# Kernel tuning notes

Measured on AMD Instinct MI355X. Metric: run time of the kernel, lower is better.

Reference implementation:

```python
import jax, jax.numpy as jnp
import numpy as np

B, T, D = 32, 2048, 256   # batch, encoder time steps, input_dim
H = 256                   # output_dim (GRU hidden)
A = 128                   # attention_dim
C = 4367                  # nb_classes
STEPS = 22                # max_out_t_steps


def setup_inputs() -> dict:
    key = jax.random.key(0)
    ks = jax.random.split(key, 11)
    s = 0.05
    return {
        "x": jax.random.normal(ks[0], (B, T, D), dtype=jnp.float32),
        # additive attention params: softmax_T(tanh(x Wx + h Wh) @ v)
        "Wx": jax.random.normal(ks[1], (D, A), dtype=jnp.float32) * s,
        "Wh": jax.random.normal(ks[2], (H, A), dtype=jnp.float32) * s,
        "v": jax.random.normal(ks[3], (A,), dtype=jnp.float32) * s,
        # torch GRUCell params
        "W_ih": jax.random.normal(ks[4], (3 * H, D), dtype=jnp.float32) * s,
        "W_hh": jax.random.normal(ks[5], (3 * H, H), dtype=jnp.float32) * s,
        "b_ih": jax.random.normal(ks[6], (3 * H,), dtype=jnp.float32) * s,
        "b_hh": jax.random.normal(ks[7], (3 * H,), dtype=jnp.float32) * s,
        # classifier
        "W_cls": jax.random.normal(ks[8], (C, H), dtype=jnp.float32) * s,
        "b_cls": jax.random.normal(ks[9], (C,), dtype=jnp.float32) * s,
    }


def reference(x, Wx, Wh, v, W_ih, W_hh, b_ih, b_hh, W_cls, b_cls):
    # dropout layers are identity in eval/reference mode
    xW = jnp.einsum("btd,da->bta", x, Wx)  # hoisted: constant across steps
    h0 = jnp.zeros((x.shape[0], H), dtype=x.dtype)

    def step(h, _):
        # additive attention over time axis
        e = jnp.einsum("bta,a->bt", jnp.tanh(xW + (h @ Wh)[:, None, :]), v)
        att = jax.nn.softmax(e, axis=1)          # [B, T]
        ctx = jnp.einsum("btd,bt->bd", x, att)   # weighted sum over T
        # torch GRUCell
        gi = ctx @ W_ih.T + b_ih                  # [B, 3H]
        gh = h @ W_hh.T + b_hh                    # [B, 3H]
        i_r, i_z, i_n = jnp.split(gi, 3, axis=1)
        h_r, h_z, h_n = jnp.split(gh, 3, axis=1)
        r = jax.nn.sigmoid(i_r + h_r)
        z = jax.nn.sigmoid(i_z + h_z)
        n = jnp.tanh(i_n + r * h_n)
        h_new = (1.0 - z) * n + z * h
        logits = h_new @ W_cls.T + b_cls          # [B, C]
        return h_new, logits

    _, outs = jax.lax.scan(step, h0, None, length=STEPS)  # [STEPS, B, C]
    return jnp.transpose(outs, (1, 0, 2))                 # [B, STEPS, C]
```

## Files before the change

### kernel.cpp

```cpp
#include <hip/hip_runtime.h>

#define BB 32
#define TT 2048
#define DD 256
#define HH 256
#define AA 128
#define CC 4367
#define CLS_LD 4480
#define NSTEPS 22
#define NCHUNK 32

typedef unsigned short ushortT;
typedef unsigned int uintT;
typedef unsigned long long u64T;
using frag8 = __attribute__((ext_vector_type(8))) short;
using f32x4 = __attribute__((ext_vector_type(4))) float;

__device__ __forceinline__ float tanh_fast(float u) {
  float e = __expf(2.0f * u);
  return 1.0f - 2.0f / (e + 1.0f);
}
__device__ __forceinline__ float sigmoid_fast(float u) {
  return 1.0f / (1.0f + __expf(-u));
}
__device__ __forceinline__ ushortT f2bf(float f) {
  unsigned int u = __float_as_uint(f);
  unsigned int r = (u + 0x7FFFu + ((u >> 16) & 1u)) >> 16;
  return (ushortT)r;
}
__device__ __forceinline__ float bf2f(ushortT v) {
  return __uint_as_float(((unsigned int)v) << 16);
}

__global__ __launch_bounds__(256) void trans_kernel(
    const float* __restrict__ Wx, const float* __restrict__ W_cls,
    float* __restrict__ WclsT, ushortT* __restrict__ WxT_bf) {
  int blk = blockIdx.x;
  __shared__ float tile[32][33];
  const int li = threadIdx.x >> 5, lj = threadIdx.x & 31;
  if (blk < 1096) {
    int i0 = (blk >> 3) * 32, j0 = (blk & 7) * 32;
#pragma unroll
    for (int k = 0; k < 4; ++k) {
      int i = i0 + li + k * 8;
      if (i < CC) tile[li + k * 8][lj] = W_cls[(size_t)i * 256 + j0 + lj];
    }
    __syncthreads();
#pragma unroll
    for (int k = 0; k < 4; ++k) {
      int j = j0 + li + k * 8, i = i0 + lj;
      if (i < CC) WclsT[(size_t)j * CLS_LD + i] = tile[lj][li + k * 8];
    }
  } else {
    blk -= 1096;
    int i0 = (blk >> 2) * 32, j0 = (blk & 3) * 32;
#pragma unroll
    for (int k = 0; k < 4; ++k)
      tile[li + k * 8][lj] = Wx[(size_t)(i0 + li + k * 8) * 128 + j0 + lj];
    __syncthreads();
#pragma unroll
    for (int k = 0; k < 4; ++k) {
      int j = j0 + li + k * 8;
      WxT_bf[(size_t)j * 256 + i0 + lj] = f2bf(tile[lj][li + k * 8]);
    }
  }
}

__global__ __launch_bounds__(256) void xw_mfma(
    const float* __restrict__ x, const ushortT* __restrict__ WxT_bf,
    ushortT* __restrict__ x_bf, ushortT* __restrict__ xWT) {
  __shared__ ushortT lds[2 * 128 * 72];
#define SX(r, c) lds[(r) * 72 + (c)]
#define SW(r, c) lds[128 * 72 + (r) * 72 + (c)]
#define ST(a, m) lds[(a) * 136 + (m)]
  const int tid = threadIdx.x;
  const int lane = tid & 63, w = tid >> 6;
  const int l15 = lane & 15, quad = lane >> 4;
  const int r0 = blockIdx.x * 128;
  const int bb = blockIdx.x >> 4, t0 = (blockIdx.x & 15) * 128;
  const int row = tid >> 1, half = tid & 1;

  f32x4 acc[2][8];
#pragma unroll
  for (int mt = 0; mt < 2; ++mt)
#pragma unroll
    for (int nt = 0; nt < 8; ++nt) acc[mt][nt] = (f32x4){0.f, 0.f, 0.f, 0.f};

  for (int kk0 = 0; kk0 < 256; kk0 += 64) {
    {
      const float4* xp = (const float4*)(x + (size_t)(r0 + row) * DD + kk0 + half * 32);
      uint4 pk[4];
#pragma unroll
      for (int i = 0; i < 4; ++i) {
        float4 f0 = xp[2 * i], f1 = xp[2 * i + 1];
        pk[i].x = (uintT)f2bf(f0.x) | ((uintT)f2bf(f0.y) << 16);
        pk[i].y = (uintT)f2bf(f0.z) | ((uintT)f2bf(f0.w) << 16);
        pk[i].z = (uintT)f2bf(f1.x) | ((uintT)f2bf(f1.y) << 16);
        pk[i].w = (uintT)f2bf(f1.z) | ((uintT)f2bf(f1.w) << 16);
      }
      uint4* sxp = (uint4*)&SX(row, half * 32);
      uint4* gxp = (uint4*)(x_bf + (size_t)(r0 + row) * DD + kk0 + half * 32);
#pragma unroll
      for (int i = 0; i < 4; ++i) { sxp[i] = pk[i]; gxp[i] = pk[i]; }
    }
    {
      const uint4* wp = (const uint4*)(WxT_bf + (size_t)row * DD + kk0 + half * 32);
      uint4* swp = (uint4*)&SW(row, half * 32);
#pragma unroll
      for (int i = 0; i < 4; ++i) swp[i] = wp[i];
    }
    __syncthreads();
#pragma unroll
    for (int kk = 0; kk < 2; ++kk) {
      frag8 a0 = *(const frag8*)&SX(w * 32 + l15, kk * 32 + quad * 8);
      frag8 a1 = *(const frag8*)&SX(w * 32 + 16 + l15, kk * 32 + quad * 8);
#pragma unroll
      for (int nt = 0; nt < 8; ++nt) {
        frag8 bf = *(const frag8*)&SW(nt * 16 + l15, kk * 32 + quad * 8);
        acc[0][nt] = __builtin_amdgcn_mfma_f32_16x16x32_bf16(a0, bf, acc[0][nt], 0, 0, 0);
        acc[1][nt] = __builtin_amdgcn_mfma_f32_16x16x32_bf16(a1, bf, acc[1][nt], 0, 0, 0);
      }
    }
    __syncthreads();
  }
#pragma unroll
  for (int mt = 0; mt < 2; ++mt)
#pragma unroll
    for (int nt = 0; nt < 8; ++nt)
#pragma unroll
      for (int r = 0; r < 4; ++r) {
        int m = w * 32 + mt * 16 + quad * 4 + r;
        int a = nt * 16 + l15;
        ST(a, m) = f2bf(acc[mt][nt][r]);
      }
  __syncthreads();
  {
    const uint4* sp = (const uint4*)&ST(row, half * 64);
    uint4* gp = (uint4*)(xWT + ((size_t)bb * AA + row) * TT + t0 + half * 64);
#pragma unroll
    for (int i = 0; i < 8; ++i) gp[i] = sp[i];
  }
#undef SX
#undef SW
#undef ST
}

__global__ __launch_bounds__(256) void gates_kernel(
    const float* __restrict__ ctx_part, const float* __restrict__ den_part,
    const float* __restrict__ hall, const float* __restrict__ W_ih,
    const float* __restrict__ W_hh, const float* __restrict__ b_ih,
    const float* __restrict__ b_hh, float* __restrict__ gi_buf,
    float* __restrict__ gh_buf, int s) {
  const int slice = blockIdx.x, b = blockIdx.y, tid = threadIdx.x;
  __shared__ __align__(16) float sctx[DD];
  __shared__ float sden;
  if (tid < 32) {
    float d = den_part[b * NCHUNK + tid];
#pragma unroll
    for (int off = 16; off > 0; off >>= 1) d += __shfl_down(d, off, 32);
    if (tid == 0) sden = d;
  }
  {
    float acc = 0.f;
#pragma unroll
    for (int c = 0; c < NCHUNK; ++c)
      acc += ctx_part[((size_t)b * NCHUNK + c) * DD + tid];
    sctx[tid] = acc;
  }
  __syncthreads();
  const float invd = 1.0f / sden;
  const int kq = tid & 15, gsub = tid >> 4;
  const float4* cp = (const float4*)sctx + kq * 4;
  const float4* hrow = (s >= 2) ? (const float4*)(hall + ((size_t)(s - 2) * BB + b) * HH) + kq * 4 : nullptr;
  float4 c4[4], h4[4];
#pragma unroll
  for (int j = 0; j < 4; ++j) {
    float4 cv = cp[j];
    c4[j].x = cv.x * invd; c4[j].y = cv.y * invd; c4[j].z = cv.z * invd; c4[j].w = cv.w * invd;
    if (hrow) h4[j] = hrow[j];
    else { h4[j].x = 0.f; h4[j].y = 0.f; h4[j].z = 0.f; h4[j].w = 0.f; }
  }
#pragma unroll
  for (int it = 0; it < 3; ++it) {
    const int g = slice * 48 + it * 16 + gsub;
    const float4* wi = (const float4*)(W_ih + (size_t)g * DD) + kq * 4;
    const float4* wh = (const float4*)(W_hh + (size_t)g * HH) + kq * 4;
    float gi = 0.f, gh = 0.f;
#pragma unroll
    for (int j = 0; j < 4; ++j) {
      float4 wv = wi[j];
      gi += c4[j].x * wv.x + c4[j].y * wv.y + c4[j].z * wv.z + c4[j].w * wv.w;
      wv = wh[j];
      gh += h4[j].x * wv.x + h4[j].y * wv.y + h4[j].z * wv.z + h4[j].w * wv.w;
    }
#pragma unroll
    for (int off = 8; off > 0; off >>= 1) {
      gi += __shfl_down(gi, off, 16);
      gh += __shfl_down(gh, off, 16);
    }
    if (kq == 0) {
      gi_buf[b * 768 + g] = gi + b_ih[g];
      gh_buf[b * 768 + g] = gh + b_hh[g];
    }
  }
}

__global__ __launch_bounds__(256) void hcomb_kernel(
    const float* __restrict__ gi_buf, const float* __restrict__ gh_buf,
    const float* __restrict__ Wh, float* __restrict__ hall,
    float* __restrict__ hWh_buf, int s) {
  const int b = blockIdx.x, as = blockIdx.y, i = threadIdx.x;
  __shared__ float sh[HH];
  __shared__ float part[8][32];
  {
    float gir = gi_buf[b * 768 + i], giz = gi_buf[b * 768 + 256 + i], gin = gi_buf[b * 768 + 512 + i];
    float ghr = gh_buf[b * 768 + i], ghz = gh_buf[b * 768 + 256 + i], ghn = gh_buf[b * 768 + 512 + i];
    float hp = (s >= 2) ? hall[((size_t)(s - 2) * BB + b) * HH + i] : 0.f;
    float r = sigmoid_fast(gir + ghr);
    float z = sigmoid_fast(giz + ghz);
    float n = tanh_fast(gin + r * ghn);
    float hv = (1.f - z) * n + z * hp;
    if (as == 0) hall[((size_t)(s - 1) * BB + b) * HH + i] = hv;
    sh[i] = hv;
  }
  __syncthreads();
  {
    const int a = i & 31, kq = i >> 5;
    const int ga = as * 32 + a;
    float acc = 0.f;
#pragma unroll
    for (int k = kq * 32; k < kq * 32 + 32; ++k)
      acc = fmaf(sh[k], Wh[k * AA + ga], acc);
    part[kq][a] = acc;
  }
  __syncthreads();
  if (i < 32) {
    float sum = part[0][i] + part[1][i] + part[2][i] + part[3][i]
              + part[4][i] + part[5][i] + part[6][i] + part[7][i];
    hWh_buf[b * AA + as * 32 + i] = sum;
  }
}

__global__ __launch_bounds__(256, 4) void att_kernel(
    const ushortT* __restrict__ x_bf, const ushortT* __restrict__ xWT_bf,
    const float* __restrict__ hWh_buf, const float* __restrict__ v,
    float* __restrict__ ctx_part, float* __restrict__ den_part) {
  const int tid = threadIdx.x;
  const int b = blockIdx.x;
  const int chunk = blockIdx.y;
  const int t0 = chunk * 64;
  __shared__ float sh_hWh[AA], sh_v[AA];
  __shared__ float sh_part[8 * 64];
  __shared__ float sh_w[64];
  __shared__ __align__(16) float sh_ctx[4 * DD];
  if (tid < AA) {
    sh_hWh[tid] = hWh_buf ? hWh_buf[b * AA + tid] : 0.f;
    sh_v[tid] = v[tid];
  }
  const int j4 = tid >> 6, dq = tid & 63;
  u64T xr[16];
  {
    const u64T* xb4 = (const u64T*)x_bf;
#pragma unroll
    for (int j = 0; j < 16; ++j)
      xr[j] = __builtin_nontemporal_load(
          &xb4[(((size_t)(b * TT + t0 + j * 4 + j4)) * DD >> 2) + dq]);
  }
  __syncthreads();
  {
    const int q = tid >> 5, tp = tid & 31;
    float p0 = 0.f, p1 = 0.f;
    const ushort2* xw2 = (const ushort2*)xWT_bf;
    const size_t base = (size_t)b * (AA * TT / 2) + (t0 >> 1) + tp;
#pragma unroll
    for (int i = 0; i < 16; ++i) {
      int a = q * 16 + i;
      ushort2 u = xw2[base + (size_t)a * (TT / 2)];
      float hwa = sh_hWh[a], va = sh_v[a];
      p0 = fmaf(tanh_fast(bf2f(u.x) + hwa), va, p0);
      p1 = fmaf(tanh_fast(bf2f(u.y) + hwa), va, p1);
    }
    sh_part[q * 64 + 2 * tp] = p0;
    sh_part[q * 64 + 2 * tp + 1] = p1;
  }
  __syncthreads();
  if (tid < 64) {
    float e = 0.f;
#pragma unroll
    for (int q = 0; q < 8; ++q) e += sh_part[q * 64 + tid];
    sh_w[tid] = __expf(e);
  }
  __syncthreads();
  {
    float4 acc = {0.f, 0.f, 0.f, 0.f};
#pragma unroll
    for (int j = 0; j < 16; ++j) {
      float w = sh_w[j * 4 + j4];
      u64T u = xr[j];
      acc.x = fmaf(w, bf2f((ushortT)(u       & 0xFFFFu)), acc.x);
      acc.y = fmaf(w, bf2f((ushortT)((u >> 16) & 0xFFFFu)), acc.y);
      acc.z = fmaf(w, bf2f((ushortT)((u >> 32) & 0xFFFFu)), acc.z);
      acc.w = fmaf(w, bf2f((ushortT)((u >> 48) & 0xFFFFu)), acc.w);
    }
    ((float4*)sh_ctx)[j4 * 64 + dq] = acc;
  }
  __syncthreads();
  {
    float sum = sh_ctx[tid] + sh_ctx[DD + tid] + sh_ctx[2 * DD + tid] + sh_ctx[3 * DD + tid];
    ctx_part[((size_t)b * NCHUNK + chunk) * DD + tid] = sum;
  }
  if (tid < 64) {
    float ds = sh_w[tid];
#pragma unroll
    for (int off = 32; off > 0; off >>= 1) ds += __shfl_down(ds, off, 64);
    if (tid == 0) den_part[b * NCHUNK + chunk] = ds;
  }
}

__global__ __launch_bounds__(256) void cls_kernel(
    const float* __restrict__ hall, const float* __restrict__ WclsT,
    const float* __restrict__ b_cls, float* __restrict__ out) {
  const int tid = threadIdx.x;
  const int c0 = blockIdx.x * 128;
  const int r0 = blockIdx.y * 32;
  const int cq = tid & 31, rg = tid >> 5;
  const int c = c0 + cq * 4;
  __shared__ __align__(16) float shh[32 * HH];
  {
    const float4* hsrc = (const float4*)(hall + (size_t)r0 * HH);
    float4* hdst = (float4*)shh;
#pragma unroll
    for (int i = 0; i < 8; ++i) hdst[tid + 256 * i] = hsrc[tid + 256 * i];
  }
  __syncthreads();
  float acc[4][4];
#pragma unroll
  for (int j = 0; j < 4; ++j)
#pragma unroll
    for (int l = 0; l < 4; ++l) acc[j][l] = 0.f;
#pragma unroll 4
  for (int k = 0; k < HH; ++k) {
    float4 w4 = *(const float4*)(WclsT + (size_t)k * CLS_LD + c);
    float h0 = shh[(rg * 4 + 0) * HH + k];
    float h1 = shh[(rg * 4 + 1) * HH + k];
    float h2 = shh[(rg * 4 + 2) * HH + k];
    float h3 = shh[(rg * 4 + 3) * HH + k];
    acc[0][0] = fmaf(h0, w4.x, acc[0][0]); acc[0][1] = fmaf(h0, w4.y, acc[0][1]);
    acc[0][2] = fmaf(h0, w4.z, acc[0][2]); acc[0][3] = fmaf(h0, w4.w, acc[0][3]);
    acc[1][0] = fmaf(h1, w4.x, acc[1][0]); acc[1][1] = fmaf(h1, w4.y, acc[1][1]);
    acc[1][2] = fmaf(h1, w4.z, acc[1][2]); acc[1][3] = fmaf(h1, w4.w, acc[1][3]);
    acc[2][0] = fmaf(h2, w4.x, acc[2][0]); acc[2][1] = fmaf(h2, w4.y, acc[2][1]);
    acc[2][2] = fmaf(h2, w4.z, acc[2][2]); acc[2][3] = fmaf(h2, w4.w, acc[2][3]);
    acc[3][0] = fmaf(h3, w4.x, acc[3][0]); acc[3][1] = fmaf(h3, w4.y, acc[3][1]);
    acc[3][2] = fmaf(h3, w4.z, acc[3][2]); acc[3][3] = fmaf(h3, w4.w, acc[3][3]);
  }
#pragma unroll
  for (int j = 0; j < 4; ++j) {
    int row = r0 + rg * 4 + j;
    int bb = row & (BB - 1), st = row >> 5;
    size_t obase = ((size_t)bb * NSTEPS + st) * CC;
#pragma unroll
    for (int l = 0; l < 4; ++l) {
      int cc = c + l;
      if (cc < CC) out[obase + cc] = acc[j][l] + b_cls[cc];
    }
  }
}

extern "C" void kernel_launch(void* const* d_in, const int* in_sizes, int n_in,
                              void* d_out, int out_size, void* d_ws, size_t ws_size,
                              hipStream_t stream) {
  const float* x     = (const float*)d_in[0];
  const float* Wx    = (const float*)d_in[1];
  const float* Wh    = (const float*)d_in[2];
  const float* v     = (const float*)d_in[3];
  const float* W_ih  = (const float*)d_in[4];
  const float* W_hh  = (const float*)d_in[5];
  const float* b_ih  = (const float*)d_in[6];
  const float* b_hh  = (const float*)d_in[7];
  const float* W_cls = (const float*)d_in[8];
  const float* b_cls = (const float*)d_in[9];
  float* out = (float*)d_out;

  float* ctx_part = (float*)d_ws;
  float* den_part = ctx_part + (size_t)BB * NCHUNK * DD;
  float* hWh_buf  = den_part + BB * NCHUNK;
  float* gi_buf   = hWh_buf + BB * AA;
  float* gh_buf   = gi_buf + BB * 768;
  float* hall     = gh_buf + BB * 768;
  float* WclsT    = hall + (size_t)NSTEPS * BB * HH;
  ushortT* WxT_bf = (ushortT*)(WclsT + (size_t)256 * CLS_LD);
  ushortT* x_bf   = WxT_bf + 128 * 256;
  ushortT* xWT    = x_bf + (size_t)BB * TT * DD;

  trans_kernel<<<1096 + 32, 256, 0, stream>>>(Wx, W_cls, WclsT, WxT_bf);
  xw_mfma<<<(BB * TT) / 128, 256, 0, stream>>>(x, WxT_bf, x_bf, xWT);

  att_kernel<<<dim3(BB, NCHUNK), 256, 0, stream>>>(x_bf, xWT, nullptr, v, ctx_part, den_part);
  for (int s = 1; s < NSTEPS; ++s) {
    gates_kernel<<<dim3(16, BB), 256, 0, stream>>>(ctx_part, den_part, hall, W_ih, W_hh,
                                                   b_ih, b_hh, gi_buf, gh_buf, s);
    hcomb_kernel<<<dim3(BB, 4), 256, 0, stream>>>(gi_buf, gh_buf, Wh, hall, hWh_buf, s);
    att_kernel<<<dim3(BB, NCHUNK), 256, 0, stream>>>(x_bf, xWT, hWh_buf, v, ctx_part, den_part);
  }
  gates_kernel<<<dim3(16, BB), 256, 0, stream>>>(ctx_part, den_part, hall, W_ih, W_hh,
                                                 b_ih, b_hh, gi_buf, gh_buf, NSTEPS);
  hcomb_kernel<<<dim3(BB, 4), 256, 0, stream>>>(gi_buf, gh_buf, Wh, hall, hWh_buf, NSTEPS);
  cls_kernel<<<dim3(35, 22), 256, 0, stream>>>(hall, WclsT, b_cls, out);
}
```

Measured before the change: 690.6 us.

## Fuse GRU combine and h·Wh projection into attention kernel; shrink classifier tiles

Removes the per-step hcomb kernel launch. Each attention block now recomputes the GRU hidden-state update and the h·Wh projection redundantly per chunk, overlapping it with its x loads. Only chunk 0 writes h back to global memory. The classifier kernel processes 16 rows per block instead of 32, doubling the grid for more parallelism. In exchange, the full 256x128 Wh matvec is recomputed in all 32 chunks per batch row, which adds redundant compute and L2 traffic.

```diff
diff --git a/kernel.cpp b/kernel.cpp
--- a/kernel.cpp
+++ b/kernel.cpp
@@ -207,44 +207,24 @@
 
 __global__ __launch_bounds__(256) void hcomb_kernel(
     const float* __restrict__ gi_buf, const float* __restrict__ gh_buf,
-    const float* __restrict__ Wh, float* __restrict__ hall,
-    float* __restrict__ hWh_buf, int s) {
-  const int b = blockIdx.x, as = blockIdx.y, i = threadIdx.x;
-  __shared__ float sh[HH];
-  __shared__ float part[8][32];
-  {
-    float gir = gi_buf[b * 768 + i], giz = gi_buf[b * 768 + 256 + i], gin = gi_buf[b * 768 + 512 + i];
-    float ghr = gh_buf[b * 768 + i], ghz = gh_buf[b * 768 + 256 + i], ghn = gh_buf[b * 768 + 512 + i];
-    float hp = (s >= 2) ? hall[((size_t)(s - 2) * BB + b) * HH + i] : 0.f;
-    float r = sigmoid_fast(gir + ghr);
-    float z = sigmoid_fast(giz + ghz);
-    float n = tanh_fast(gin + r * ghn);
-    float hv = (1.f - z) * n + z * hp;
-    if (as == 0) hall[((size_t)(s - 1) * BB + b) * HH + i] = hv;
-    sh[i] = hv;
-  }
-  __syncthreads();
-  {
-    const int a = i & 31, kq = i >> 5;
-    const int ga = as * 32 + a;
-    float acc = 0.f;
-#pragma unroll
-    for (int k = kq * 32; k < kq * 32 + 32; ++k)
-      acc = fmaf(sh[k], Wh[k * AA + ga], acc);
-    part[kq][a] = acc;
-  }
-  __syncthreads();
-  if (i < 32) {
-    float sum = part[0][i] + part[1][i] + part[2][i] + part[3][i]
-              + part[4][i] + part[5][i] + part[6][i] + part[7][i];
-    hWh_buf[b * AA + as * 32 + i] = sum;
-  }
+    float* __restrict__ hall, int s) {
+  const int b = blockIdx.x, i = threadIdx.x;
+  float gir = gi_buf[b * 768 + i], giz = gi_buf[b * 768 + 256 + i], gin = gi_buf[b * 768 + 512 + i];
+  float ghr = gh_buf[b * 768 + i], ghz = gh_buf[b * 768 + 256 + i], ghn = gh_buf[b * 768 + 512 + i];
+  float hp = (s >= 2) ? hall[((size_t)(s - 2) * BB + b) * HH + i] : 0.f;
+  float r = sigmoid_fast(gir + ghr);
+  float z = sigmoid_fast(giz + ghz);
+  float n = tanh_fast(gin + r * ghn);
+  float hv = (1.f - z) * n + z * hp;
+  hall[((size_t)(s - 1) * BB + b) * HH + i] = hv;
 }
 
 __global__ __launch_bounds__(256, 4) void att_kernel(
     const ushortT* __restrict__ x_bf, const ushortT* __restrict__ xWT_bf,
-    const float* __restrict__ hWh_buf, const float* __restrict__ v,
-    float* __restrict__ ctx_part, float* __restrict__ den_part) {
+    const float* __restrict__ gi_buf, const float* __restrict__ gh_buf,
+    const float* __restrict__ Wh, float* __restrict__ hall,
+    const float* __restrict__ v, float* __restrict__ ctx_part,
+    float* __restrict__ den_part, int s) {
   const int tid = threadIdx.x;
   const int b = blockIdx.x;
   const int chunk = blockIdx.y;
@@ -253,10 +233,9 @@
   __shared__ float sh_part[8 * 64];
   __shared__ float sh_w[64];
   __shared__ __align__(16) float sh_ctx[4 * DD];
-  if (tid < AA) {
-    sh_hWh[tid] = hWh_buf ? hWh_buf[b * AA + tid] : 0.f;
-    sh_v[tid] = v[tid];
-  }
+  __shared__ __align__(16) float sh_h[HH];
+  __shared__ float hpart[2][AA];
+  if (tid < AA) sh_v[tid] = v[tid];
   const int j4 = tid >> 6, dq = tid & 63;
   u64T xr[16];
   {
@@ -265,6 +244,30 @@
     for (int j = 0; j < 16; ++j)
       xr[j] = __builtin_nontemporal_load(
           &xb4[(((size_t)(b * TT + t0 + j * 4 + j4)) * DD >> 2) + dq]);
+  }
+  if (s >= 1) {
+    float gir = gi_buf[b * 768 + tid], giz = gi_buf[b * 768 + 256 + tid], gin = gi_buf[b * 768 + 512 + tid];
+    float ghr = gh_buf[b * 768 + tid], ghz = gh_buf[b * 768 + 256 + tid], ghn = gh_buf[b * 768 + 512 + tid];
+    float hp = (s >= 2) ? hall[((size_t)(s - 2) * BB + b) * HH + tid] : 0.f;
+    float r = sigmoid_fast(gir + ghr);
+    float z = sigmoid_fast(giz + ghz);
+    float n = tanh_fast(gin + r * ghn);
+    float hv = (1.f - z) * n + z * hp;
+    if (chunk == 0) hall[((size_t)(s - 1) * BB + b) * HH + tid] = hv;
+    sh_h[tid] = hv;
+    __syncthreads();
+    {
+      const int a = tid & 127, kh = tid >> 7;
+      float acc = 0.f;
+#pragma unroll 8
+      for (int k = kh * 128; k < kh * 128 + 128; ++k)
+        acc = fmaf(sh_h[k], Wh[k * AA + a], acc);
+      hpart[kh][a] = acc;
+    }
+    __syncthreads();
+    if (tid < AA) sh_hWh[tid] = hpart[0][tid] + hpart[1][tid];
+  } else {
+    if (tid < AA) sh_hWh[tid] = 0.f;
   }
   __syncthreads();
   {
@@ -322,41 +325,35 @@
     const float* __restrict__ b_cls, float* __restrict__ out) {
   const int tid = threadIdx.x;
   const int c0 = blockIdx.x * 128;
-  const int r0 = blockIdx.y * 32;
+  const int r0 = blockIdx.y * 16;
   const int cq = tid & 31, rg = tid >> 5;
   const int c = c0 + cq * 4;
-  __shared__ __align__(16) float shh[32 * HH];
+  __shared__ __align__(16) float shh[16 * HH];
   {
     const float4* hsrc = (const float4*)(hall + (size_t)r0 * HH);
     float4* hdst = (float4*)shh;
 #pragma unroll
-    for (int i = 0; i < 8; ++i) hdst[tid + 256 * i] = hsrc[tid + 256 * i];
-  }
-  __syncthreads();
-  float acc[4][4];
-#pragma unroll
-  for (int j = 0; j < 4; ++j)
+    for (int i = 0; i < 4; ++i) hdst[tid + 256 * i] = hsrc[tid + 256 * i];
+  }
+  __syncthreads();
+  float acc[2][4];
+#pragma unroll
+  for (int j = 0; j < 2; ++j)
 #pragma unroll
     for (int l = 0; l < 4; ++l) acc[j][l] = 0.f;
 #pragma unroll 4
   for (int k = 0; k < HH; ++k) {
     float4 w4 = *(const float4*)(WclsT + (size_t)k * CLS_LD + c);
-    float h0 = shh[(rg * 4 + 0) * HH + k];
-    float h1 = shh[(rg * 4 + 1) * HH + k];
-    float h2 = shh[(rg * 4 + 2) * HH + k];
-    float h3 = shh[(rg * 4 + 3) * HH + k];
+    float h0 = shh[(rg * 2 + 0) * HH + k];
+    float h1 = shh[(rg * 2 + 1) * HH + k];
     acc[0][0] = fmaf(h0, w4.x, acc[0][0]); acc[0][1] = fmaf(h0, w4.y, acc[0][1]);
     acc[0][2] = fmaf(h0, w4.z, acc[0][2]); acc[0][3] = fmaf(h0, w4.w, acc[0][3]);
     acc[1][0] = fmaf(h1, w4.x, acc[1][0]); acc[1][1] = fmaf(h1, w4.y, acc[1][1]);
     acc[1][2] = fmaf(h1, w4.z, acc[1][2]); acc[1][3] = fmaf(h1, w4.w, acc[1][3]);
-    acc[2][0] = fmaf(h2, w4.x, acc[2][0]); acc[2][1] = fmaf(h2, w4.y, acc[2][1]);
-    acc[2][2] = fmaf(h2, w4.z, acc[2][2]); acc[2][3] = fmaf(h2, w4.w, acc[2][3]);
-    acc[3][0] = fmaf(h3, w4.x, acc[3][0]); acc[3][1] = fmaf(h3, w4.y, acc[3][1]);
-    acc[3][2] = fmaf(h3, w4.z, acc[3][2]); acc[3][3] = fmaf(h3, w4.w, acc[3][3]);
-  }
-#pragma unroll
-  for (int j = 0; j < 4; ++j) {
-    int row = r0 + rg * 4 + j;
+  }
+#pragma unroll
+  for (int j = 0; j < 2; ++j) {
+    int row = r0 + rg * 2 + j;
     int bb = row & (BB - 1), st = row >> 5;
     size_t obase = ((size_t)bb * NSTEPS + st) * CC;
 #pragma unroll
@@ -384,8 +381,7 @@
 
   float* ctx_part = (float*)d_ws;
   float* den_part = ctx_part + (size_t)BB * NCHUNK * DD;
-  float* hWh_buf  = den_part + BB * NCHUNK;
-  float* gi_buf   = hWh_buf + BB * AA;
+  float* gi_buf   = den_part + BB * NCHUNK;
   float* gh_buf   = gi_buf + BB * 768;
   float* hall     = gh_buf + BB * 768;
   float* WclsT    = hall + (size_t)NSTEPS * BB * HH;
@@ -396,15 +392,16 @@
   trans_kernel<<<1096 + 32, 256, 0, stream>>>(Wx, W_cls, WclsT, WxT_bf);
   xw_mfma<<<(BB * TT) / 128, 256, 0, stream>>>(x, WxT_bf, x_bf, xWT);
 
-  att_kernel<<<dim3(BB, NCHUNK), 256, 0, stream>>>(x_bf, xWT, nullptr, v, ctx_part, den_part);
+  att_kernel<<<dim3(BB, NCHUNK), 256, 0, stream>>>(x_bf, xWT, nullptr, nullptr,
+                                                   Wh, hall, v, ctx_part, den_part, 0);
   for (int s = 1; s < NSTEPS; ++s) {
     gates_kernel<<<dim3(16, BB), 256, 0, stream>>>(ctx_part, den_part, hall, W_ih, W_hh,
                                                    b_ih, b_hh, gi_buf, gh_buf, s);
-    hcomb_kernel<<<dim3(BB, 4), 256, 0, stream>>>(gi_buf, gh_buf, Wh, hall, hWh_buf, s);
-    att_kernel<<<dim3(BB, NCHUNK), 256, 0, stream>>>(x_bf, xWT, hWh_buf, v, ctx_part, den_part);
+    att_kernel<<<dim3(BB, NCHUNK), 256, 0, stream>>>(x_bf, xWT, gi_buf, gh_buf,
+                                                     Wh, hall, v, ctx_part, den_part, s);
   }
   gates_kernel<<<dim3(16, BB), 256, 0, stream>>>(ctx_part, den_part, hall, W_ih, W_hh,
                                                  b_ih, b_hh, gi_buf, gh_buf, NSTEPS);
-  hcomb_kernel<<<dim3(BB, 4), 256, 0, stream>>>(gi_buf, gh_buf, Wh, hall, hWh_buf, NSTEPS);
-  cls_kernel<<<dim3(35, 22), 256, 0, stream>>>(hall, WclsT, b_cls, out);
-}
+  hcomb_kernel<<<BB, 256, 0, stream>>>(gi_buf, gh_buf, hall, NSTEPS);
+  cls_kernel<<<dim3(35, 44), 256, 0, stream>>>(hall, WclsT, b_cls, out);
+}
```

Result: slower. 754.9 us (+9.3%).
